# Optimization experiments

Hardware: AMD Instinct MI355X
Metric: run time of the kernel (lower is better)

Reference implementation:

```python
import jax, jax.numpy as jnp
import numpy as np

NEG_SLOPE = 0.2  # leaky_relu slope used by standard GAT attention


def _gat_layer(h, src, dst, W, a_src, a_dst, gru, n_nodes):
    """One gated multi-head GAT layer.
    h: [N, Din]; W: [H, Din, D]; a_src/a_dst: [H, D]; gru: None or (Wih,Whh,bih,bhh).
    Heads are merged by mean so output is [N, D].
    """
    Wh = jnp.einsum('nd,hdo->nho', h, W)                      # [N, H, D]
    es = jnp.einsum('nho,ho->nh', Wh, a_src)                  # [N, H]
    ed = jnp.einsum('nho,ho->nh', Wh, a_dst)                  # [N, H]
    e = jax.nn.leaky_relu(es[src] + ed[dst], NEG_SLOPE)       # [E, H]
    # edge softmax over each destination's in-neighborhood (segment softmax)
    m = jax.ops.segment_max(e, dst, num_segments=n_nodes)     # [N, H]
    w = jnp.exp(e - m[dst])                                   # [E, H]
    denom = jax.ops.segment_sum(w, dst, num_segments=n_nodes) # [N, H]
    alpha = w / denom[dst]                                    # [E, H]
    # gather-source / scatter-add aggregation
    agg = jax.ops.segment_sum(alpha[:, :, None] * Wh[src], dst,
                              num_segments=n_nodes)           # [N, H, D]
    out = jax.nn.elu(agg.mean(axis=1))                        # [N, D] (head-mean merge)
    if gru is not None:
        Wih, Whh, bih, bhh = gru
        gi = out @ Wih.T + bih                                # [N, 3D]
        gh = h @ Whh.T + bhh                                  # [N, 3D]
        ir, iz, in_ = jnp.split(gi, 3, axis=-1)
        hr, hz, hn = jnp.split(gh, 3, axis=-1)
        r = jax.nn.sigmoid(ir + hr)
        z = jax.nn.sigmoid(iz + hz)
        n = jnp.tanh(in_ + r * hn)
        out = (1.0 - z) * n + z * h                           # GRU-gated residual update
    return out


def setup_inputs() -> dict:
    N, E, D, H, OUT = 20000, 320000, 128, 4, 1
    key = jax.random.key(0)
    ks = jax.random.split(key, 24)
    sd = 1.0 / np.sqrt(D)
    inp = {
        'h': jax.random.normal(ks[0], (N, D), jnp.float32),
        'edge_index': jax.random.randint(ks[1], (2, E), 0, N, jnp.int64),
    }
    # GAT layers: layer1-3 have H heads, layer4 has 1 head
    heads = [H, H, H, 1]
    for i, hh in enumerate(heads, start=1):
        inp[f'W{i}'] = jax.random.normal(ks[2 + 3 * i], (hh, D, D), jnp.float32) * sd
        inp[f'as{i}'] = jax.random.normal(ks[3 + 3 * i], (hh, D), jnp.float32) * 0.1
        inp[f'ad{i}'] = jax.random.normal(ks[4 + 3 * i], (hh, D), jnp.float32) * 0.1
    # shared GRUSubLayer(hidden_dim) parameters (torch GRUCell layout)
    inp['Wih'] = jax.random.normal(ks[18], (3 * D, D), jnp.float32) * sd
    inp['Whh'] = jax.random.normal(ks[19], (3 * D, D), jnp.float32) * sd
    inp['bih'] = jnp.zeros((3 * D,), jnp.float32)
    inp['bhh'] = jnp.zeros((3 * D,), jnp.float32)
    # output head
    inp['W5'] = jax.random.normal(ks[20], (D, OUT), jnp.float32) * sd
    inp['b5'] = jnp.zeros((OUT,), jnp.float32)
    return inp


def reference(h, edge_index, W1, as1, ad1, W2, as2, ad2, W3, as3, ad3,
              W4, as4, ad4, Wih, Whh, bih, bhh, W5, b5):
    N = h.shape[0]
    src, dst = edge_index[0], edge_index[1]
    gru = (Wih, Whh, bih, bhh)
    h = _gat_layer(h, src, dst, W1, as1, ad1, None, N)   # require_gru=False
    h = _gat_layer(h, src, dst, W2, as2, ad2, gru, N)
    h = _gat_layer(h, src, dst, W3, as3, ad3, gru, N)
    h = _gat_layer(h, src, dst, W4, as4, ad4, gru, N)    # single head
    return jax.nn.sigmoid(h @ W5 + b5)                   # [N, out_dim]
```

## Files before the change

### kernel.cpp

```cpp
#include <hip/hip_runtime.h>
#include <math.h>

#define D 128

typedef __attribute__((ext_vector_type(8))) short bf16x8;
typedef __attribute__((ext_vector_type(4))) float f32x4;

__device__ __forceinline__ float sigmoidf_(float x) { return 1.f / (1.f + __expf(-x)); }
__device__ __forceinline__ float bf2f(unsigned short u) { return __uint_as_float(((unsigned)u) << 16); }
__device__ __forceinline__ float u2f_lo(unsigned u) { return __uint_as_float(u << 16); }
__device__ __forceinline__ float u2f_hi(unsigned u) { return __uint_as_float(u & 0xffff0000u); }
__device__ __forceinline__ unsigned short f2b(float f) {
  unsigned u = __float_as_uint(f);
  return (unsigned short)((u + 0x7fffu + ((u >> 16) & 1u)) >> 16);
}
__device__ __forceinline__ float leaky_(float v) { return v > 0.f ? v : 0.2f * v; }

__device__ __forceinline__ void pack_post_elem(const float* __restrict__ W,
                                               unsigned short* __restrict__ Bp, int i, float scale) {
  int j = i & 7;
  int lane = (i >> 3) & 63;
  int rest = i >> 9;
  int db = rest & 7;
  int kb = rest >> 3;
  int k = kb * 32 + ((lane >> 4) << 3) + j;
  int d = db * 16 + (lane & 15);
  int h = k >> 7, kk = k & 127;
  Bp[i] = f2b(W[((size_t)h * 128 + kk) * 128 + d] * scale);
}
__device__ __forceinline__ void pack_gru_elem(const float* __restrict__ S,
                                              unsigned short* __restrict__ Bp, int i) {
  int j = i & 7;
  int lane = (i >> 3) & 63;
  int rest = i >> 9;
  int db = rest % 24;
  int kb = rest / 24;
  int k = kb * 32 + ((lane >> 4) << 3) + j;
  int col = db * 16 + (lane & 15);
  Bp[i] = f2b(S[(size_t)col * 128 + k]);
}

__global__ void __launch_bounds__(256) k_prep(const float* __restrict__ h0, unsigned short* __restrict__ h0b,
                                              const float* __restrict__ W1, const float* __restrict__ W2,
                                              const float* __restrict__ W3, const float* __restrict__ W4,
                                              const float* __restrict__ Wih, const float* __restrict__ Whh,
                                              unsigned short* __restrict__ B1, unsigned short* __restrict__ B2,
                                              unsigned short* __restrict__ B3, unsigned short* __restrict__ B4,
                                              unsigned short* __restrict__ Bih, unsigned short* __restrict__ Bhh,
                                              const float* __restrict__ as1, const float* __restrict__ ad1,
                                              const float* __restrict__ as2, const float* __restrict__ ad2,
                                              const float* __restrict__ as3, const float* __restrict__ ad3,
                                              const float* __restrict__ as4, const float* __restrict__ ad4,
                                              unsigned short* __restrict__ Pp1, float* __restrict__ Pf2,
                                              float* __restrict__ Pf3, float* __restrict__ Pf4,
                                              const int* __restrict__ dst, int* __restrict__ deg,
                                              int N, int E) {
  int i = blockIdx.x * 256 + threadIdx.x;
  const int NH = N * 128;
  if (i < NH) {
    h0b[i] = f2b(h0[i]);
    return;
  }
  i -= NH;
  if (i < 311296) {
    if (i < 65536) pack_post_elem(W1, B1, i, 0.25f);
    else if (i < 131072) pack_post_elem(W2, B2, i - 65536, 0.25f);
    else if (i < 196608) pack_post_elem(W3, B3, i - 131072, 0.25f);
    else if (i < 212992) pack_post_elem(W4, B4, i - 196608, 1.0f);
    else if (i < 262144) pack_gru_elem(Wih, Bih, i - 212992);
    else pack_gru_elem(Whh, Bhh, i - 262144);
    return;
  }
  i -= 311296;
  if (i < 2048) {
    int j = i & 7;
    int lane = (i >> 3) & 63;
    int kb = i >> 9;
    int k = kb * 32 + ((lane >> 4) << 3) + j;
    int col = lane & 15;
    float val = 0.f;
    if (col < 8) {
      int c = col >= 4;
      int h = c ? (col - 4) : col;
      const float* wrow = W1 + ((size_t)h * 128 + k) * 128;
      const float* av = (c ? ad1 : as1) + (size_t)h * 128;
      for (int d2 = 0; d2 < 128; ++d2) val += wrow[d2] * av[d2];
    }
    Pp1[i] = f2b(val);
    return;
  }
  i -= 2048;
  if (i < 3072) {
    int layer = i >> 10;
    int qq = i & 1023;
    int k = qq >> 3;
    int slot = qq & 7;
    const float *W, *as_, *ad_;
    float* out;
    int H;
    if (layer == 0) { W = W2; as_ = as2; ad_ = ad2; out = Pf2; H = 4; }
    else if (layer == 1) { W = W3; as_ = as3; ad_ = ad3; out = Pf3; H = 4; }
    else { W = W4; as_ = as4; ad_ = ad4; out = Pf4; H = 1; }
    int h = slot & 3;
    bool isEd = slot >= 4;
    float val = 0.f;
    if (h < H) {
      const float* wrow = W + ((size_t)h * 128 + k) * 128;
      const float* av = (isEd ? ad_ : as_) + (size_t)h * 128;
      for (int d2 = 0; d2 < 128; ++d2) val += wrow[d2] * av[d2];
    }
    out[qq] = val;
    return;
  }
  i -= 3072;
  if (i < E) atomicAdd(&deg[dst[i]], 1);
}

__global__ void __launch_bounds__(256) k_esed(const unsigned short* __restrict__ hb,
                                              const unsigned short* __restrict__ Pp,
                                              float* __restrict__ es, float* __restrict__ ed, int N) {
  const int w = threadIdx.x >> 6;
  const int lane = threadIdx.x & 63;
  const int r = lane & 15, g = lane >> 4;
  const int n0 = blockIdx.x * 64 + w * 16;
  f32x4 acc = (f32x4)0.f;
  const int koff = g << 3;
#pragma unroll
  for (int kb = 0; kb < 4; ++kb) {
    int row = min(n0 + r, N - 1);
    bf16x8 a = *(const bf16x8*)&hb[(size_t)row * 128 + kb * 32 + koff];
    bf16x8 b = *(const bf16x8*)&Pp[((size_t)(kb * 64) + lane) * 8];
    acc = __builtin_amdgcn_mfma_f32_16x16x32_bf16(a, b, acc, 0, 0, 0);
  }
  const int rbase = n0 + g * 4;
#pragma unroll
  for (int i = 0; i < 4; ++i) {
    int row = rbase + i;
    if (row < N) {
      if (r < 4) es[(size_t)row * 4 + r] = acc[i];
      else if (r < 8) ed[(size_t)row * 4 + (r - 4)] = acc[i];
    }
  }
}

__global__ void __launch_bounds__(1024) k_scan(const int* __restrict__ deg, int* __restrict__ rowptr,
                                               int* __restrict__ fill, int N) {
  __shared__ int part[1024];
  const int tid = threadIdx.x;
  const int chunk = (N + 1023) / 1024;
  const int b = tid * chunk;
  const int e = min(N, b + chunk);
  int s = 0;
  for (int i = b; i < e; ++i) s += deg[i];
  part[tid] = s;
  __syncthreads();
  for (int off = 1; off < 1024; off <<= 1) {
    int v = (tid >= off) ? part[tid - off] : 0;
    __syncthreads();
    part[tid] += v;
    __syncthreads();
  }
  int run = (tid == 0) ? 0 : part[tid - 1];
  for (int i = b; i < e; ++i) {
    rowptr[i] = run;
    fill[i] = run;
    run += deg[i];
  }
  if (b < N && e == N) rowptr[N] = run;
}

__global__ void __launch_bounds__(256) k_scatter(const int* __restrict__ src, const int* __restrict__ dst,
                                                 int* __restrict__ fill, int* __restrict__ srcs, int E) {
  int e = blockIdx.x * 256 + threadIdx.x;
  if (e >= E) return;
  int pos = atomicAdd(&fill[dst[e]], 1);
  srcs[pos] = src[e];
}

template <int H>
__global__ void __launch_bounds__(256) k_edge_gather(const int* __restrict__ rowptr,
                                                     const int* __restrict__ srcs,
                                                     const float* __restrict__ es,
                                                     const float* __restrict__ ed,
                                                     const unsigned short* __restrict__ hb,
                                                     unsigned short* __restrict__ tb, int N) {
  __shared__ unsigned s_off[4][64];
  __shared__ float s_af[4][64][H == 1 ? 1 : 4];
  const int wid = threadIdx.x >> 6;
  const int t = blockIdx.x * 4 + wid;
  if (t >= N) return;
  const int lane = threadIdx.x & 63;
  const int q = lane & 15;
  const int eg = lane >> 4;
  const int b0 = rowptr[t];
  const int deg = rowptr[t + 1] - b0;
  unsigned short* trow = tb + (size_t)t * (H * 128);
  if (deg == 0) {
    if (lane < 16) {
#pragma unroll
      for (int h = 0; h < H; ++h)
        *(uint4*)&trow[h * 128 + q * 8] = make_uint4(0u, 0u, 0u, 0u);
    }
    return;
  }
  float edv[H];
#pragma unroll
  for (int h = 0; h < H; ++h) edv[h] = ed[(size_t)t * H + h];

  float acc[H][8];
#pragma unroll
  for (int h = 0; h < H; ++h)
#pragma unroll
    for (int j = 0; j < 8; ++j) acc[h][j] = 0.f;
  const char* hbase = (const char*)hb + q * 16;

  if (deg <= 64) {
    const bool act = lane < deg;
    int s = 0;
    float vv[H];
    if (act) {
      s = srcs[b0 + lane];
      if constexpr (H == 4) {
        float4 ev = *(const float4*)&es[(size_t)s * 4];
        vv[0] = leaky_(ev.x + edv[0]);
        vv[1] = leaky_(ev.y + edv[1]);
        vv[2] = leaky_(ev.z + edv[2]);
        vv[3] = leaky_(ev.w + edv[3]);
      } else {
        vv[0] = leaky_(es[s] + edv[0]);
      }
    } else {
#pragma unroll
      for (int h = 0; h < H; ++h) vv[h] = -1e30f;
    }
    float mv[H];
#pragma unroll
    for (int h = 0; h < H; ++h) mv[h] = vv[h];
#pragma unroll
    for (int off = 32; off; off >>= 1)
#pragma unroll
      for (int h = 0; h < H; ++h) mv[h] = fmaxf(mv[h], __shfl_xor(mv[h], off));
    float e[H], den[H];
#pragma unroll
    for (int h = 0; h < H; ++h) {
      e[h] = act ? __expf(vv[h] - mv[h]) : 0.f;
      den[h] = e[h];
    }
#pragma unroll
    for (int off = 32; off; off >>= 1)
#pragma unroll
      for (int h = 0; h < H; ++h) den[h] += __shfl_xor(den[h], off);
    s_off[wid][lane] = act ? ((unsigned)s << 8) : 0u;
#pragma unroll
    for (int h = 0; h < H; ++h) s_af[wid][lane][h] = e[h] * (1.f / den[h]);
    const int steps = (deg + 3) >> 2;
#pragma unroll 4
    for (int e2 = 0; e2 < steps; ++e2) {
      const int ei = e2 * 4 + eg;
      unsigned off = s_off[wid][ei];
      float af[H];
      if constexpr (H == 4) {
        float4 a4 = *(const float4*)&s_af[wid][ei][0];
        af[0] = a4.x; af[1] = a4.y; af[2] = a4.z; af[3] = a4.w;
      } else {
        af[0] = s_af[wid][ei][0];
      }
      uint4 v = *(const uint4*)(hbase + off);
      float vf[8] = {u2f_lo(v.x), u2f_hi(v.x), u2f_lo(v.y), u2f_hi(v.y),
                     u2f_lo(v.z), u2f_hi(v.z), u2f_lo(v.w), u2f_hi(v.w)};
#pragma unroll
      for (int h = 0; h < H; ++h)
#pragma unroll
        for (int j = 0; j < 8; ++j) acc[h][j] += af[h] * vf[j];
    }
  } else {
    float m[H], den[H], vreg[H];
    int sreg = 0;
#pragma unroll
    for (int h = 0; h < H; ++h) {
      m[h] = -1e30f;
      den[h] = 0.f;
      vreg[h] = -1e30f;
    }
    for (int i = lane; i < deg; i += 64) {
      int s = srcs[b0 + i];
      float vv[H];
      if constexpr (H == 4) {
        float4 ev = *(const float4*)&es[(size_t)s * 4];
        vv[0] = ev.x + edv[0];
        vv[1] = ev.y + edv[1];
        vv[2] = ev.z + edv[2];
        vv[3] = ev.w + edv[3];
      } else {
        vv[0] = es[s] + edv[0];
      }
#pragma unroll
      for (int h = 0; h < H; ++h) {
        float v = leaky_(vv[h]);
        vv[h] = v;
        float nm = fmaxf(m[h], v);
        den[h] = den[h] * __expf(m[h] - nm) + __expf(v - nm);
        m[h] = nm;
      }
      if (i == lane) {
        sreg = s;
#pragma unroll
        for (int h = 0; h < H; ++h) vreg[h] = vv[h];
      }
    }
#pragma unroll
    for (int off = 32; off; off >>= 1) {
#pragma unroll
      for (int h = 0; h < H; ++h) {
        float om = __shfl_xor(m[h], off);
        float od = __shfl_xor(den[h], off);
        float nm = fmaxf(m[h], om);
        den[h] = den[h] * __expf(m[h] - nm) + od * __expf(om - nm);
        m[h] = nm;
      }
    }
    float rden[H];
#pragma unroll
    for (int h = 0; h < H; ++h) rden[h] = 1.f / den[h];
    for (int c0 = 0; c0 < deg; c0 += 64) {
      const int ce = min(64, deg - c0);
      if (c0 == 0) {
        bool ok = lane < deg;
        s_off[wid][lane] = ok ? ((unsigned)sreg << 8) : 0u;
#pragma unroll
        for (int h = 0; h < H; ++h)
          s_af[wid][lane][h] = ok ? (__expf(vreg[h] - m[h]) * rden[h]) : 0.f;
      } else {
        int i = c0 + lane;
        bool ok = i < deg;
        int s = ok ? srcs[b0 + i] : 0;
        s_off[wid][lane] = ok ? ((unsigned)s << 8) : 0u;
        float af[H];
#pragma unroll
        for (int h = 0; h < H; ++h) af[h] = 0.f;
        if (ok) {
          float vv[H];
          if constexpr (H == 4) {
            float4 ev = *(const float4*)&es[(size_t)s * 4];
            vv[0] = ev.x + edv[0];
            vv[1] = ev.y + edv[1];
            vv[2] = ev.z + edv[2];
            vv[3] = ev.w + edv[3];
          } else {
            vv[0] = es[s] + edv[0];
          }
#pragma unroll
          for (int h = 0; h < H; ++h)
            af[h] = __expf(leaky_(vv[h]) - m[h]) * rden[h];
        }
#pragma unroll
        for (int h = 0; h < H; ++h) s_af[wid][lane][h] = af[h];
      }
      const int steps = (ce + 3) >> 2;
#pragma unroll 4
      for (int e2 = 0; e2 < steps; ++e2) {
        const int ei = e2 * 4 + eg;
        unsigned off = s_off[wid][ei];
        float af[H];
        if constexpr (H == 4) {
          float4 a4 = *(const float4*)&s_af[wid][ei][0];
          af[0] = a4.x; af[1] = a4.y; af[2] = a4.z; af[3] = a4.w;
        } else {
          af[0] = s_af[wid][ei][0];
        }
        uint4 v = *(const uint4*)(hbase + off);
        float vf[8] = {u2f_lo(v.x), u2f_hi(v.x), u2f_lo(v.y), u2f_hi(v.y),
                       u2f_lo(v.z), u2f_hi(v.z), u2f_lo(v.w), u2f_hi(v.w)};
#pragma unroll
        for (int h = 0; h < H; ++h)
#pragma unroll
          for (int j = 0; j < 8; ++j) acc[h][j] += af[h] * vf[j];
      }
    }
  }
#pragma unroll
  for (int h = 0; h < H; ++h)
#pragma unroll
    for (int j = 0; j < 8; ++j) {
      acc[h][j] += __shfl_xor(acc[h][j], 16);
      acc[h][j] += __shfl_xor(acc[h][j], 32);
    }
  if (lane < 16) {
#pragma unroll
    for (int h = 0; h < H; ++h) {
      uint4 pk;
      pk.x = (unsigned)f2b(acc[h][0]) | ((unsigned)f2b(acc[h][1]) << 16);
      pk.y = (unsigned)f2b(acc[h][2]) | ((unsigned)f2b(acc[h][3]) << 16);
      pk.z = (unsigned)f2b(acc[h][4]) | ((unsigned)f2b(acc[h][5]) << 16);
      pk.w = (unsigned)f2b(acc[h][6]) | ((unsigned)f2b(acc[h][7]) << 16);
      *(uint4*)&trow[h * 128 + q * 8] = pk;
    }
  }
}

__global__ void __launch_bounds__(256) k_post1(const unsigned short* __restrict__ tb,
                                               const unsigned short* __restrict__ Bp,
                                               float* __restrict__ houtf,
                                               unsigned short* __restrict__ houtb,
                                               const float* __restrict__ Pf,
                                               float* __restrict__ es, float* __restrict__ ed) {
  __shared__ float s_pr[16][8][4];
  const int n0 = blockIdx.x * 16;
  const int w = threadIdx.x >> 6;
  const int lane = threadIdx.x & 63;
  const int r = lane & 15, g = lane >> 4;
  f32x4 acc[2];
  acc[0] = (f32x4)0.f;
  acc[1] = (f32x4)0.f;
  const int koff = g << 3;
#pragma unroll
  for (int kb = 0; kb < 16; ++kb) {
    bf16x8 a = *(const bf16x8*)&tb[(size_t)(n0 + r) * 512 + kb * 32 + koff];
#pragma unroll
    for (int t = 0; t < 2; ++t) {
      bf16x8 b = *(const bf16x8*)&Bp[((size_t)(kb * 8 + w * 2 + t) * 64 + lane) * 8];
      acc[t] = __builtin_amdgcn_mfma_f32_16x16x32_bf16(a, b, acc[t], 0, 0, 0);
    }
  }
  float ps[4][8];
#pragma unroll
  for (int i = 0; i < 4; ++i)
#pragma unroll
    for (int c = 0; c < 8; ++c) ps[i][c] = 0.f;
#pragma unroll
  for (int t = 0; t < 2; ++t) {
    const int col = (w * 2 + t) * 16 + r;
    float4 pj0 = *(const float4*)&Pf[col * 8];
    float4 pj1 = *(const float4*)&Pf[col * 8 + 4];
#pragma unroll
    for (int i = 0; i < 4; ++i) {
      const int row = n0 + g * 4 + i;
      float o = acc[t][i];
      o = o > 0.f ? o : expm1f(o);
      houtf[(size_t)row * 128 + col] = o;
      houtb[(size_t)row * 128 + col] = f2b(o);
      ps[i][0] += o * pj0.x; ps[i][1] += o * pj0.y;
      ps[i][2] += o * pj0.z; ps[i][3] += o * pj0.w;
      ps[i][4] += o * pj1.x; ps[i][5] += o * pj1.y;
      ps[i][6] += o * pj1.z; ps[i][7] += o * pj1.w;
    }
  }
#pragma unroll
  for (int off = 1; off < 16; off <<= 1)
#pragma unroll
    for (int i = 0; i < 4; ++i)
#pragma unroll
      for (int c = 0; c < 8; ++c) ps[i][c] += __shfl_xor(ps[i][c], off);
  if (r == 0) {
#pragma unroll
    for (int i = 0; i < 4; ++i)
#pragma unroll
      for (int c = 0; c < 8; ++c) s_pr[g * 4 + i][c][w] = ps[i][c];
  }
  __syncthreads();
  if (threadIdx.x < 128) {
    int row = threadIdx.x >> 3;
    int c = threadIdx.x & 7;
    float val = s_pr[row][c][0] + s_pr[row][c][1] + s_pr[row][c][2] + s_pr[row][c][3];
    int gr = n0 + row;
    if (c < 4) es[(size_t)gr * 4 + c] = val;
    else ed[(size_t)gr * 4 + (c - 4)] = val;
  }
}

template <int KD, int MODE>
__global__ void __launch_bounds__(256) k_postgru(const unsigned short* __restrict__ tb,
                                                 const unsigned short* __restrict__ Bp,
                                                 const unsigned short* __restrict__ hb,
                                                 const float* __restrict__ hf,
                                                 const unsigned short* __restrict__ Bih,
                                                 const unsigned short* __restrict__ Bhh,
                                                 const float* __restrict__ bih,
                                                 const float* __restrict__ bhh,
                                                 float* __restrict__ houtf,
                                                 unsigned short* __restrict__ houtb,
                                                 const float* __restrict__ Pf,
                                                 float* __restrict__ es, float* __restrict__ ed, int Hn,
                                                 const float* __restrict__ W5,
                                                 const float* __restrict__ b5,
                                                 float* __restrict__ out) {
  __shared__ unsigned short xs[16][136];
  __shared__ float s_pr[16][8][4];
  const int n0 = blockIdx.x * 16;
  const int w = threadIdx.x >> 6;
  const int lane = threadIdx.x & 63;
  const int r = lane & 15, g = lane >> 4;
  const int koff = g << 3;
  {
    f32x4 acc[2];
    acc[0] = (f32x4)0.f;
    acc[1] = (f32x4)0.f;
#pragma unroll
    for (int kb = 0; kb < KD / 32; ++kb) {
      bf16x8 a = *(const bf16x8*)&tb[(size_t)(n0 + r) * KD + kb * 32 + koff];
#pragma unroll
      for (int t = 0; t < 2; ++t) {
        bf16x8 b = *(const bf16x8*)&Bp[((size_t)(kb * 8 + w * 2 + t) * 64 + lane) * 8];
        acc[t] = __builtin_amdgcn_mfma_f32_16x16x32_bf16(a, b, acc[t], 0, 0, 0);
      }
    }
#pragma unroll
    for (int t = 0; t < 2; ++t) {
      const int col = (w * 2 + t) * 16 + r;
#pragma unroll
      for (int i = 0; i < 4; ++i) {
        float o = acc[t][i];
        o = o > 0.f ? o : expm1f(o);
        xs[g * 4 + i][col] = f2b(o);
      }
    }
  }
  __syncthreads();
  const int qbase = w * 2;
  f32x4 ai[3][2], ah[3][2];
#pragma unroll
  for (int p = 0; p < 3; ++p)
#pragma unroll
    for (int t = 0; t < 2; ++t) {
      ai[p][t] = (f32x4)0.f;
      ah[p][t] = (f32x4)0.f;
    }
#pragma unroll
  for (int kb = 0; kb < 4; ++kb) {
    bf16x8 ax = *(const bf16x8*)&xs[r][kb * 32 + koff];
    bf16x8 ahr = *(const bf16x8*)&hb[(size_t)(n0 + r) * 128 + kb * 32 + koff];
#pragma unroll
    for (int p = 0; p < 3; ++p) {
#pragma unroll
      for (int t = 0; t < 2; ++t) {
        const int ct = p * 8 + qbase + t;
        bf16x8 bi = *(const bf16x8*)&Bih[((size_t)(kb * 24 + ct) * 64 + lane) * 8];
        bf16x8 bh = *(const bf16x8*)&Bhh[((size_t)(kb * 24 + ct) * 64 + lane) * 8];
        ai[p][t] = __builtin_amdgcn_mfma_f32_16x16x32_bf16(ax, bi, ai[p][t], 0, 0, 0);
        ah[p][t] = __builtin_amdgcn_mfma_f32_16x16x32_bf16(ahr, bh, ah[p][t], 0, 0, 0);
      }
    }
  }
  if constexpr (MODE == 0) {
    float ps[4][8];
#pragma unroll
    for (int i = 0; i < 4; ++i)
#pragma unroll
      for (int c = 0; c < 8; ++c) ps[i][c] = 0.f;
#pragma unroll
    for (int t = 0; t < 2; ++t) {
      const int j = (qbase + t) * 16 + r;
      const float bir = bih[j], biz = bih[128 + j], bin = bih[256 + j];
      const float bhr = bhh[j], bhz = bhh[128 + j], bhn = bhh[256 + j];
      float4 pj0 = *(const float4*)&Pf[j * 8];
      float4 pj1 = *(const float4*)&Pf[j * 8 + 4];
#pragma unroll
      for (int i = 0; i < 4; ++i) {
        const int row = n0 + g * 4 + i;
        float rr = sigmoidf_(ai[0][t][i] + bir + ah[0][t][i] + bhr);
        float z = sigmoidf_(ai[1][t][i] + biz + ah[1][t][i] + bhz);
        float nn = tanhf(ai[2][t][i] + bin + rr * (ah[2][t][i] + bhn));
        float hp = hf[(size_t)row * 128 + j];
        float o = (1.f - z) * nn + z * hp;
        houtf[(size_t)row * 128 + j] = o;
        houtb[(size_t)row * 128 + j] = f2b(o);
        ps[i][0] += o * pj0.x; ps[i][1] += o * pj0.y;
        ps[i][2] += o * pj0.z; ps[i][3] += o * pj0.w;
        ps[i][4] += o * pj1.x; ps[i][5] += o * pj1.y;
        ps[i][6] += o * pj1.z; ps[i][7] += o * pj1.w;
      }
    }
#pragma unroll
    for (int off = 1; off < 16; off <<= 1)
#pragma unroll
      for (int i = 0; i < 4; ++i)
#pragma unroll
        for (int c = 0; c < 8; ++c) ps[i][c] += __shfl_xor(ps[i][c], off);
    if (r == 0) {
#pragma unroll
      for (int i = 0; i < 4; ++i)
#pragma unroll
        for (int c = 0; c < 8; ++c) s_pr[g * 4 + i][c][w] = ps[i][c];
    }
    __syncthreads();
    if (threadIdx.x < 128) {
      int row = threadIdx.x >> 3;
      int c = threadIdx.x & 7;
      float val = s_pr[row][c][0] + s_pr[row][c][1] + s_pr[row][c][2] + s_pr[row][c][3];
      int gr = n0 + row;
      if (c < Hn) es[(size_t)gr * Hn + c] = val;
      else if (c >= 4 && c < 4 + Hn) ed[(size_t)gr * Hn + (c - 4)] = val;
    }
  } else {
    float pfin[4] = {0.f, 0.f, 0.f, 0.f};
#pragma unroll
    for (int t = 0; t < 2; ++t) {
      const int j = (qbase + t) * 16 + r;
      const float bir = bih[j], biz = bih[128 + j], bin = bih[256 + j];
      const float bhr = bhh[j], bhz = bhh[128 + j], bhn = bhh[256 + j];
      const float w5 = W5[j];
#pragma unroll
      for (int i = 0; i < 4; ++i) {
        const int row = n0 + g * 4 + i;
        float rr = sigmoidf_(ai[0][t][i] + bir + ah[0][t][i] + bhr);
        float z = sigmoidf_(ai[1][t][i] + biz + ah[1][t][i] + bhz);
        float nn = tanhf(ai[2][t][i] + bin + rr * (ah[2][t][i] + bhn));
        float hp = hf[(size_t)row * 128 + j];
        float o = (1.f - z) * nn + z * hp;
        pfin[i] += o * w5;
      }
    }
#pragma unroll
    for (int off = 1; off < 16; off <<= 1)
#pragma unroll
      for (int i = 0; i < 4; ++i) pfin[i] += __shfl_xor(pfin[i], off);
    if (r == 0) {
#pragma unroll
      for (int i = 0; i < 4; ++i) s_pr[g * 4 + i][0][w] = pfin[i];
    }
    __syncthreads();
    if (threadIdx.x < 16) {
      float s = s_pr[threadIdx.x][0][0] + s_pr[threadIdx.x][0][1] +
                s_pr[threadIdx.x][0][2] + s_pr[threadIdx.x][0][3] + b5[0];
      out[n0 + threadIdx.x] = sigmoidf_(s);
    }
  }
}

extern "C" void kernel_launch(void* const* d_in, const int* in_sizes, int n_in,
                              void* d_out, int out_size, void* d_ws, size_t ws_size,
                              hipStream_t stream) {
  const float* h0 = (const float*)d_in[0];
  const int* ei = (const int*)d_in[1];
  const float* W1 = (const float*)d_in[2];
  const float* as1 = (const float*)d_in[3];
  const float* ad1 = (const float*)d_in[4];
  const float* W2 = (const float*)d_in[5];
  const float* as2 = (const float*)d_in[6];
  const float* ad2 = (const float*)d_in[7];
  const float* W3 = (const float*)d_in[8];
  const float* as3 = (const float*)d_in[9];
  const float* ad3 = (const float*)d_in[10];
  const float* W4 = (const float*)d_in[11];
  const float* as4 = (const float*)d_in[12];
  const float* ad4 = (const float*)d_in[13];
  const float* Wih = (const float*)d_in[14];
  const float* Whh = (const float*)d_in[15];
  const float* bih = (const float*)d_in[16];
  const float* bhh = (const float*)d_in[17];
  const float* W5 = (const float*)d_in[18];
  const float* b5 = (const float*)d_in[19];

  const int N = in_sizes[0] / D;
  const int E = in_sizes[1] / 2;
  const int* src = ei;
  const int* dst = ei + E;

  float* ws = (float*)d_ws;
  unsigned short* tb = (unsigned short*)ws;
  float* hA = ws + (size_t)N * 256;
  float* hB = hA + (size_t)N * 128;
  float* es = hB + (size_t)N * 128;
  float* ed = es + (size_t)N * 4;
  unsigned short* h0b = (unsigned short*)(ed + (size_t)N * 4);
  unsigned short* hAb = h0b + (size_t)N * 128;
  unsigned short* hBb = hAb + (size_t)N * 128;
  unsigned short* B1 = hBb + (size_t)N * 128;
  unsigned short* B2 = B1 + 65536;
  unsigned short* B3 = B2 + 65536;
  unsigned short* B4 = B3 + 65536;
  unsigned short* Bih = B4 + 16384;
  unsigned short* Bhh = Bih + 49152;
  unsigned short* Pp1 = Bhh + 49152;
  float* Pf2 = (float*)(Pp1 + 2048);
  float* Pf3 = Pf2 + 1024;
  float* Pf4 = Pf3 + 1024;
  int* deg = (int*)(Pf4 + 1024);
  int* rowptr = deg + N;
  int* fill = rowptr + N + 1;
  int* srcs = fill + N;

  hipMemsetAsync(deg, 0, (size_t)N * 4, stream);
  {
    const int total = N * 128 + 311296 + 2048 + 3072 + E;
    k_prep<<<(total + 255) / 256, 256, 0, stream>>>(
        h0, h0b, W1, W2, W3, W4, Wih, Whh, B1, B2, B3, B4, Bih, Bhh,
        as1, ad1, as2, ad2, as3, ad3, as4, ad4, Pp1, Pf2, Pf3, Pf4, dst, deg, N, E);
  }
  k_scan<<<1, 1024, 0, stream>>>(deg, rowptr, fill, N);
  k_scatter<<<(E + 255) / 256, 256, 0, stream>>>(src, dst, fill, srcs, E);

  const int gES = (N + 63) / 64;
  const int gE = (N + 3) / 4;
  const int gP = N / 16;

  k_esed<<<gES, 256, 0, stream>>>(h0b, Pp1, es, ed, N);
  k_edge_gather<4><<<gE, 256, 0, stream>>>(rowptr, srcs, es, ed, h0b, tb, N);
  k_post1<<<gP, 256, 0, stream>>>(tb, B1, hA, hAb, Pf2, es, ed);
  k_edge_gather<4><<<gE, 256, 0, stream>>>(rowptr, srcs, es, ed, hAb, tb, N);
  k_postgru<512, 0><<<gP, 256, 0, stream>>>(tb, B2, hAb, hA, Bih, Bhh, bih, bhh, hB, hBb,
                                            Pf3, es, ed, 4, nullptr, nullptr, nullptr);
  k_edge_gather<4><<<gE, 256, 0, stream>>>(rowptr, srcs, es, ed, hBb, tb, N);
  k_postgru<512, 0><<<gP, 256, 0, stream>>>(tb, B3, hBb, hB, Bih, Bhh, bih, bhh, hA, hAb,
                                            Pf4, es, ed, 1, nullptr, nullptr, nullptr);
  k_edge_gather<1><<<gE, 256, 0, stream>>>(rowptr, srcs, es, ed, hAb, tb, N);
  k_postgru<128, 1><<<gP, 256, 0, stream>>>(tb, B4, hAb, hA, Bih, Bhh, bih, bhh,
                                            nullptr, nullptr, nullptr, nullptr, nullptr, 0,
                                            W5, b5, (float*)d_out);
}
```

Measured before the change: 306.2 us.

## Use half-wave per destination node in edge gather and merge scatter with es/ed

The edge-gather kernel now assigns 32 lanes to each destination node (8 nodes per block) instead of a full 64-lane wave. Average degree is about 16, so the previous layout left many lanes idle. The accumulation is rewritten with float2 vectors so the compiler can emit packed FMA, and the cross-lane reduction drops one shuffle step. Separately, the CSR scatter and the initial es/ed MFMA projection are merged into one launch with block-range dispatch, saving a kernel launch. The cost is that nodes with degree above 32 fall to the slower chunked path more often.

```diff
diff --git a/kernel.cpp b/kernel.cpp
--- a/kernel.cpp
+++ b/kernel.cpp
@@ -5,6 +5,7 @@
 
 typedef __attribute__((ext_vector_type(8))) short bf16x8;
 typedef __attribute__((ext_vector_type(4))) float f32x4;
+typedef __attribute__((ext_vector_type(2))) float f32x2;
 
 __device__ __forceinline__ float sigmoidf_(float x) { return 1.f / (1.f + __expf(-x)); }
 __device__ __forceinline__ float bf2f(unsigned short u) { return __uint_as_float(((unsigned)u) << 16); }
@@ -116,33 +117,6 @@
   if (i < E) atomicAdd(&deg[dst[i]], 1);
 }
 
-__global__ void __launch_bounds__(256) k_esed(const unsigned short* __restrict__ hb,
-                                              const unsigned short* __restrict__ Pp,
-                                              float* __restrict__ es, float* __restrict__ ed, int N) {
-  const int w = threadIdx.x >> 6;
-  const int lane = threadIdx.x & 63;
-  const int r = lane & 15, g = lane >> 4;
-  const int n0 = blockIdx.x * 64 + w * 16;
-  f32x4 acc = (f32x4)0.f;
-  const int koff = g << 3;
-#pragma unroll
-  for (int kb = 0; kb < 4; ++kb) {
-    int row = min(n0 + r, N - 1);
-    bf16x8 a = *(const bf16x8*)&hb[(size_t)row * 128 + kb * 32 + koff];
-    bf16x8 b = *(const bf16x8*)&Pp[((size_t)(kb * 64) + lane) * 8];
-    acc = __builtin_amdgcn_mfma_f32_16x16x32_bf16(a, b, acc, 0, 0, 0);
-  }
-  const int rbase = n0 + g * 4;
-#pragma unroll
-  for (int i = 0; i < 4; ++i) {
-    int row = rbase + i;
-    if (row < N) {
-      if (r < 4) es[(size_t)row * 4 + r] = acc[i];
-      else if (r < 8) ed[(size_t)row * 4 + (r - 4)] = acc[i];
-    }
-  }
-}
-
 __global__ void __launch_bounds__(1024) k_scan(const int* __restrict__ deg, int* __restrict__ rowptr,
                                                int* __restrict__ fill, int N) {
   __shared__ int part[1024];
@@ -169,12 +143,43 @@
   if (b < N && e == N) rowptr[N] = run;
 }
 
-__global__ void __launch_bounds__(256) k_scatter(const int* __restrict__ src, const int* __restrict__ dst,
-                                                 int* __restrict__ fill, int* __restrict__ srcs, int E) {
-  int e = blockIdx.x * 256 + threadIdx.x;
-  if (e >= E) return;
-  int pos = atomicAdd(&fill[dst[e]], 1);
-  srcs[pos] = src[e];
+__global__ void __launch_bounds__(256) k_scatter_esed(const int* __restrict__ src, const int* __restrict__ dst,
+                                                      int* __restrict__ fill, int* __restrict__ srcs, int E,
+                                                      const unsigned short* __restrict__ hb,
+                                                      const unsigned short* __restrict__ Pp,
+                                                      float* __restrict__ es, float* __restrict__ ed,
+                                                      int N, int nS) {
+  if ((int)blockIdx.x < nS) {
+    int e = blockIdx.x * 256 + threadIdx.x;
+    if (e < E) {
+      int pos = atomicAdd(&fill[dst[e]], 1);
+      srcs[pos] = src[e];
+    }
+    return;
+  }
+  const int blk = blockIdx.x - nS;
+  const int w = threadIdx.x >> 6;
+  const int lane = threadIdx.x & 63;
+  const int r = lane & 15, g = lane >> 4;
+  const int n0 = blk * 64 + w * 16;
+  f32x4 acc = (f32x4)0.f;
+  const int koff = g << 3;
+#pragma unroll
+  for (int kb = 0; kb < 4; ++kb) {
+    int row = min(n0 + r, N - 1);
+    bf16x8 a = *(const bf16x8*)&hb[(size_t)row * 128 + kb * 32 + koff];
+    bf16x8 b = *(const bf16x8*)&Pp[((size_t)(kb * 64) + lane) * 8];
+    acc = __builtin_amdgcn_mfma_f32_16x16x32_bf16(a, b, acc, 0, 0, 0);
+  }
+  const int rbase = n0 + g * 4;
+#pragma unroll
+  for (int i = 0; i < 4; ++i) {
+    int row = rbase + i;
+    if (row < N) {
+      if (r < 4) es[(size_t)row * 4 + r] = acc[i];
+      else if (r < 8) ed[(size_t)row * 4 + (r - 4)] = acc[i];
+    }
+  }
 }
 
 template <int H>
@@ -184,19 +189,19 @@
                                                      const float* __restrict__ ed,
                                                      const unsigned short* __restrict__ hb,
                                                      unsigned short* __restrict__ tb, int N) {
-  __shared__ unsigned s_off[4][64];
-  __shared__ float s_af[4][64][H == 1 ? 1 : 4];
-  const int wid = threadIdx.x >> 6;
-  const int t = blockIdx.x * 4 + wid;
+  __shared__ __align__(16) unsigned s_off[8][32];
+  __shared__ __align__(16) float s_af[8][32][H == 1 ? 1 : 4];
+  const int slot = threadIdx.x >> 5;
+  const int t = blockIdx.x * 8 + slot;
   if (t >= N) return;
-  const int lane = threadIdx.x & 63;
-  const int q = lane & 15;
-  const int eg = lane >> 4;
+  const int l = threadIdx.x & 31;
+  const int q = l & 15;
+  const int eg = l >> 4;
   const int b0 = rowptr[t];
   const int deg = rowptr[t + 1] - b0;
   unsigned short* trow = tb + (size_t)t * (H * 128);
   if (deg == 0) {
-    if (lane < 16) {
+    if (l < 16) {
 #pragma unroll
       for (int h = 0; h < H; ++h)
         *(uint4*)&trow[h * 128 + q * 8] = make_uint4(0u, 0u, 0u, 0u);
@@ -207,19 +212,19 @@
 #pragma unroll
   for (int h = 0; h < H; ++h) edv[h] = ed[(size_t)t * H + h];
 
-  float acc[H][8];
+  f32x2 acc[H][4];
 #pragma unroll
   for (int h = 0; h < H; ++h)
 #pragma unroll
-    for (int j = 0; j < 8; ++j) acc[h][j] = 0.f;
+    for (int j = 0; j < 4; ++j) acc[h][j] = (f32x2)0.f;
   const char* hbase = (const char*)hb + q * 16;
 
-  if (deg <= 64) {
-    const bool act = lane < deg;
+  if (deg <= 32) {
+    const bool act = l < deg;
     int s = 0;
     float vv[H];
     if (act) {
-      s = srcs[b0 + lane];
+      s = srcs[b0 + l];
       if constexpr (H == 4) {
         float4 ev = *(const float4*)&es[(size_t)s * 4];
         vv[0] = leaky_(ev.x + edv[0]);
@@ -237,7 +242,7 @@
 #pragma unroll
     for (int h = 0; h < H; ++h) mv[h] = vv[h];
 #pragma unroll
-    for (int off = 32; off; off >>= 1)
+    for (int off = 16; off; off >>= 1)
 #pragma unroll
       for (int h = 0; h < H; ++h) mv[h] = fmaxf(mv[h], __shfl_xor(mv[h], off));
     float e[H], den[H];
@@ -247,31 +252,37 @@
       den[h] = e[h];
     }
 #pragma unroll
-    for (int off = 32; off; off >>= 1)
+    for (int off = 16; off; off >>= 1)
 #pragma unroll
       for (int h = 0; h < H; ++h) den[h] += __shfl_xor(den[h], off);
-    s_off[wid][lane] = act ? ((unsigned)s << 8) : 0u;
-#pragma unroll
-    for (int h = 0; h < H; ++h) s_af[wid][lane][h] = e[h] * (1.f / den[h]);
-    const int steps = (deg + 3) >> 2;
+    s_off[slot][l] = act ? ((unsigned)s << 8) : 0u;
+#pragma unroll
+    for (int h = 0; h < H; ++h) s_af[slot][l][h] = e[h] * (1.f / den[h]);
+    const int steps = (deg + 1) >> 1;
 #pragma unroll 4
     for (int e2 = 0; e2 < steps; ++e2) {
-      const int ei = e2 * 4 + eg;
-      unsigned off = s_off[wid][ei];
+      const int ei = e2 * 2 + eg;
+      unsigned off = s_off[slot][ei];
       float af[H];
       if constexpr (H == 4) {
-        float4 a4 = *(const float4*)&s_af[wid][ei][0];
+        float4 a4 = *(const float4*)&s_af[slot][ei][0];
         af[0] = a4.x; af[1] = a4.y; af[2] = a4.z; af[3] = a4.w;
       } else {
-        af[0] = s_af[wid][ei][0];
+        af[0] = s_af[slot][ei][0];
       }
       uint4 v = *(const uint4*)(hbase + off);
-      float vf[8] = {u2f_lo(v.x), u2f_hi(v.x), u2f_lo(v.y), u2f_hi(v.y),
-                     u2f_lo(v.z), u2f_hi(v.z), u2f_lo(v.w), u2f_hi(v.w)};
-#pragma unroll
-      for (int h = 0; h < H; ++h)
-#pragma unroll
-        for (int j = 0; j < 8; ++j) acc[h][j] += af[h] * vf[j];
+      f32x2 vf0 = {u2f_lo(v.x), u2f_hi(v.x)};
+      f32x2 vf1 = {u2f_lo(v.y), u2f_hi(v.y)};
+      f32x2 vf2 = {u2f_lo(v.z), u2f_hi(v.z)};
+      f32x2 vf3 = {u2f_lo(v.w), u2f_hi(v.w)};
+#pragma unroll
+      for (int h = 0; h < H; ++h) {
+        f32x2 a2 = {af[h], af[h]};
+        acc[h][0] += a2 * vf0;
+        acc[h][1] += a2 * vf1;
+        acc[h][2] += a2 * vf2;
+        acc[h][3] += a2 * vf3;
+      }
     }
   } else {
     float m[H], den[H], vreg[H];
@@ -282,7 +293,7 @@
       den[h] = 0.f;
       vreg[h] = -1e30f;
     }
-    for (int i = lane; i < deg; i += 64) {
+    for (int i = l; i < deg; i += 32) {
       int s = srcs[b0 + i];
       float vv[H];
       if constexpr (H == 4) {
@@ -302,14 +313,14 @@
         den[h] = den[h] * __expf(m[h] - nm) + __expf(v - nm);
         m[h] = nm;
       }
-      if (i == lane) {
+      if (i == l) {
         sreg = s;
 #pragma unroll
         for (int h = 0; h < H; ++h) vreg[h] = vv[h];
       }
     }
 #pragma unroll
-    for (int off = 32; off; off >>= 1) {
+    for (int off = 16; off; off >>= 1) {
 #pragma unroll
       for (int h = 0; h < H; ++h) {
         float om = __shfl_xor(m[h], off);
@@ -322,19 +333,19 @@
     float rden[H];
 #pragma unroll
     for (int h = 0; h < H; ++h) rden[h] = 1.f / den[h];
-    for (int c0 = 0; c0 < deg; c0 += 64) {
-      const int ce = min(64, deg - c0);
+    for (int c0 = 0; c0 < deg; c0 += 32) {
+      const int ce = min(32, deg - c0);
       if (c0 == 0) {
-        bool ok = lane < deg;
-        s_off[wid][lane] = ok ? ((unsigned)sreg << 8) : 0u;
+        bool ok = l < deg;
+        s_off[slot][l] = ok ? ((unsigned)sreg << 8) : 0u;
 #pragma unroll
         for (int h = 0; h < H; ++h)
-          s_af[wid][lane][h] = ok ? (__expf(vreg[h] - m[h]) * rden[h]) : 0.f;
+          s_af[slot][l][h] = ok ? (__expf(vreg[h] - m[h]) * rden[h]) : 0.f;
       } else {
-        int i = c0 + lane;
+        int i = c0 + l;
         bool ok = i < deg;
         int s = ok ? srcs[b0 + i] : 0;
-        s_off[wid][lane] = ok ? ((unsigned)s << 8) : 0u;
+        s_off[slot][l] = ok ? ((unsigned)s << 8) : 0u;
         float af[H];
 #pragma unroll
         for (int h = 0; h < H; ++h) af[h] = 0.f;
@@ -354,45 +365,51 @@
             af[h] = __expf(leaky_(vv[h]) - m[h]) * rden[h];
         }
 #pragma unroll
-        for (int h = 0; h < H; ++h) s_af[wid][lane][h] = af[h];
-      }
-      const int steps = (ce + 3) >> 2;
+        for (int h = 0; h < H; ++h) s_af[slot][l][h] = af[h];
+      }
+      const int steps = (ce + 1) >> 1;
 #pragma unroll 4
       for (int e2 = 0; e2 < steps; ++e2) {
-        const int ei = e2 * 4 + eg;
-        unsigned off = s_off[wid][ei];
+        const int ei = e2 * 2 + eg;
+        unsigned off = s_off[slot][ei];
         float af[H];
         if constexpr (H == 4) {
-          float4 a4 = *(const float4*)&s_af[wid][ei][0];
+          float4 a4 = *(const float4*)&s_af[slot][ei][0];
           af[0] = a4.x; af[1] = a4.y; af[2] = a4.z; af[3] = a4.w;
         } else {
-          af[0] = s_af[wid][ei][0];
+          af[0] = s_af[slot][ei][0];
         }
         uint4 v = *(const uint4*)(hbase + off);
-        float vf[8] = {u2f_lo(v.x), u2f_hi(v.x), u2f_lo(v.y), u2f_hi(v.y),
-                       u2f_lo(v.z), u2f_hi(v.z), u2f_lo(v.w), u2f_hi(v.w)};
-#pragma unroll
-        for (int h = 0; h < H; ++h)
-#pragma unroll
-          for (int j = 0; j < 8; ++j) acc[h][j] += af[h] * vf[j];
+        f32x2 vf0 = {u2f_lo(v.x), u2f_hi(v.x)};
+        f32x2 vf1 = {u2f_lo(v.y), u2f_hi(v.y)};
+        f32x2 vf2 = {u2f_lo(v.z), u2f_hi(v.z)};
+        f32x2 vf3 = {u2f_lo(v.w), u2f_hi(v.w)};
+#pragma unroll
+        for (int h = 0; h < H; ++h) {
+          f32x2 a2 = {af[h], af[h]};
+          acc[h][0] += a2 * vf0;
+          acc[h][1] += a2 * vf1;
+          acc[h][2] += a2 * vf2;
+          acc[h][3] += a2 * vf3;
+        }
       }
     }
   }
 #pragma unroll
   for (int h = 0; h < H; ++h)
 #pragma unroll
-    for (int j = 0; j < 8; ++j) {
-      acc[h][j] += __shfl_xor(acc[h][j], 16);
-      acc[h][j] += __shfl_xor(acc[h][j], 32);
-    }
-  if (lane < 16) {
+    for (int j = 0; j < 4; ++j) {
+      acc[h][j].x += __shfl_xor(acc[h][j].x, 16);
+      acc[h][j].y += __shfl_xor(acc[h][j].y, 16);
+    }
+  if (l < 16) {
 #pragma unroll
     for (int h = 0; h < H; ++h) {
       uint4 pk;
-      pk.x = (unsigned)f2b(acc[h][0]) | ((unsigned)f2b(acc[h][1]) << 16);
-      pk.y = (unsigned)f2b(acc[h][2]) | ((unsigned)f2b(acc[h][3]) << 16);
-      pk.z = (unsigned)f2b(acc[h][4]) | ((unsigned)f2b(acc[h][5]) << 16);
-      pk.w = (unsigned)f2b(acc[h][6]) | ((unsigned)f2b(acc[h][7]) << 16);
+      pk.x = (unsigned)f2b(acc[h][0].x) | ((unsigned)f2b(acc[h][0].y) << 16);
+      pk.y = (unsigned)f2b(acc[h][1].x) | ((unsigned)f2b(acc[h][1].y) << 16);
+      pk.z = (unsigned)f2b(acc[h][2].x) | ((unsigned)f2b(acc[h][2].y) << 16);
+      pk.w = (unsigned)f2b(acc[h][3].x) | ((unsigned)f2b(acc[h][3].y) << 16);
       *(uint4*)&trow[h * 128 + q * 8] = pk;
     }
   }
@@ -688,13 +705,16 @@
         as1, ad1, as2, ad2, as3, ad3, as4, ad4, Pp1, Pf2, Pf3, Pf4, dst, deg, N, E);
   }
   k_scan<<<1, 1024, 0, stream>>>(deg, rowptr, fill, N);
-  k_scatter<<<(E + 255) / 256, 256, 0, stream>>>(src, dst, fill, srcs, E);
-
-  const int gES = (N + 63) / 64;
-  const int gE = (N + 3) / 4;
+  {
+    const int nS = (E + 255) / 256;
+    const int nE = (N + 63) / 64;
+    k_scatter_esed<<<nS + nE, 256, 0, stream>>>(src, dst, fill, srcs, E,
+                                                h0b, Pp1, es, ed, N, nS);
+  }
+
+  const int gE = (N + 7) / 8;
   const int gP = N / 16;
 
-  k_esed<<<gES, 256, 0, stream>>>(h0b, Pp1, es, ed, N);
   k_edge_gather<4><<<gE, 256, 0, stream>>>(rowptr, srcs, es, ed, h0b, tb, N);
   k_post1<<<gP, 256, 0, stream>>>(tb, B1, hA, hAb, Pf2, es, ed);
   k_edge_gather<4><<<gE, 256, 0, stream>>>(rowptr, srcs, es, ed, hAb, tb, N);
```

After: 267.0 us. 12.8% less time.
